# Optimization experiments

Measured on AMD Instinct MI355X. Metric: run time of the kernel, lower is better.

## Reference

```python
import jax, jax.numpy as jnp
import numpy as np

N = 100000   # nodes
E = 1600000  # edges
G = 512      # graphs in batch
F_IN = 30
H = 128
EPS = 1e-5   # BatchNorm1d default eps


def setup_inputs() -> dict:
    key = jax.random.key(0)
    ks = jax.random.split(key, 16)
    x = jax.random.normal(ks[0], (N, F_IN), dtype=jnp.float32)
    edge_index = jax.random.randint(ks[1], (2, E), 0, N, dtype=jnp.int64)
    batch = jnp.sort(jax.random.randint(ks[2], (N,), 0, G, dtype=jnp.int64))
    d = {"x": x, "edge_index": edge_index, "batch": batch}
    dims = [(F_IN, H), (H, H), (H, H)]
    for i, (din, dout) in enumerate(dims):
        d[f"W{i}"] = jax.random.normal(ks[3 + i], (din, dout), dtype=jnp.float32) * (1.0 / np.sqrt(din))
        d[f"b{i}"] = jnp.zeros((dout,), dtype=jnp.float32)
        d[f"g{i}"] = jnp.ones((dout,), dtype=jnp.float32)   # BN gamma
        d[f"bt{i}"] = jnp.zeros((dout,), dtype=jnp.float32)  # BN beta
    d["HW1"] = jax.random.normal(ks[9], (H, 64), dtype=jnp.float32) * (1.0 / np.sqrt(H))
    d["Hb1"] = jnp.zeros((64,), dtype=jnp.float32)
    d["HW2"] = jax.random.normal(ks[10], (64, 1), dtype=jnp.float32) * 0.125
    d["Hb2"] = jnp.zeros((1,), dtype=jnp.float32)
    return d


def _bn(x, gamma, beta):
    # training-mode BatchNorm1d over node dim, biased variance (as torch uses for normalization)
    mu = jnp.mean(x, axis=0)
    var = jnp.mean(jnp.square(x - mu), axis=0)
    return (x - mu) * jax.lax.rsqrt(var + EPS) * gamma + beta


def reference(x, edge_index, batch, W0, b0, g0, bt0, W1, b1, g1, bt1, W2, b2, g2, bt2, HW1, Hb1, HW2, Hb2):
    # GCNConv: add self-loops, symmetric D^{-1/2}(A+I)D^{-1/2} normalization
    loop = jnp.arange(N, dtype=edge_index.dtype)
    src = jnp.concatenate([edge_index[0], loop])  # [E+N]
    dst = jnp.concatenate([edge_index[1], loop])
    deg = jax.ops.segment_sum(jnp.ones(src.shape, jnp.float32), dst, num_segments=N)
    dinv = jax.lax.rsqrt(jnp.maximum(deg, 1.0))  # deg >= 1 due to self-loops
    norm = (dinv[src] * dinv[dst])[:, None]      # [E+N, 1]

    for W, b, g, bt in ((W0, b0, g0, bt0), (W1, b1, g1, bt1), (W2, b2, g2, bt2)):
        h = x @ W                                           # [N, H]
        agg = jax.ops.segment_sum(h[src] * norm, dst, num_segments=N) + b
        x = jnp.maximum(_bn(agg, g, bt), 0.0)               # BN + ReLU (dropout = identity here)

    # global_mean_pool over graph ids
    counts = jax.ops.segment_sum(jnp.ones((N,), jnp.float32), batch, num_segments=G)
    pooled = jax.ops.segment_sum(x, batch, num_segments=G) / jnp.maximum(counts, 1.0)[:, None]

    h = jnp.maximum(pooled @ HW1 + Hb1, 0.0)
    return (h @ HW2 + Hb2).squeeze(-1)  # [G]
```

## Files before the change

### kernel.cpp

```cpp
#include <hip/hip_runtime.h>

#define BN_EPS 1e-5f
#define BSH 8

typedef __attribute__((ext_vector_type(8))) short bf16x8;
typedef __attribute__((ext_vector_type(4))) float f32x4;

__device__ inline float bfhi(unsigned int v) { return __uint_as_float(v & 0xFFFF0000u); }
__device__ inline float bflo(unsigned int v) { return __uint_as_float(v << 16); }
__device__ inline unsigned short f2bf(float f) {
  unsigned int u = __float_as_uint(f);
  u += 0x7FFFu + ((u >> 16) & 1u);
  return (unsigned short)(u >> 16);
}
__device__ inline unsigned int pack2bf(float lo, float hi) {
  return (unsigned int)f2bf(lo) | ((unsigned int)f2bf(hi) << 16);
}

__global__ void k_prep(const int* __restrict__ src, const int* __restrict__ dst,
                       int* __restrict__ gcur, uint2* __restrict__ sedge,
                       int NB, int CAP, int E, int BB,
                       const float* __restrict__ x, const float* __restrict__ W0,
                       const float* __restrict__ W1, const float* __restrict__ W2,
                       unsigned short* __restrict__ xb, unsigned short* __restrict__ Wt0,
                       unsigned short* __restrict__ Wt1, unsigned short* __restrict__ Wt2,
                       int n) {
  if ((int)blockIdx.x < BB) {
    __shared__ int lh[512], rb[512];
    int tid = threadIdx.x;
    for (int i = tid; i < NB; i += 256) lh[i] = 0;
    __syncthreads();
    int base = blockIdx.x * 8192;
    int lim = min(8192, E - base);
    for (int i = tid; i < lim; i += 256)
      atomicAdd(&lh[dst[base + i] >> BSH], 1);
    __syncthreads();
    for (int i = tid; i < NB; i += 256) {
      int c = lh[i];
      rb[i] = c ? atomicAdd(&gcur[i], c) : 0;
      lh[i] = 0;
    }
    __syncthreads();
    for (int i = tid; i < lim; i += 256) {
      int d = dst[base + i];
      int s = src[base + i];
      int b = d >> BSH;
      int pos = rb[b] + atomicAdd(&lh[b], 1);
      if (pos < CAP) {
        uint2 v; v.x = (unsigned int)s; v.y = (unsigned int)d;
        sedge[(size_t)b * CAP + pos] = v;
      }
    }
  } else {
    int t0 = (((int)blockIdx.x - BB) * 256 + (int)threadIdx.x) * 4;
#pragma unroll
    for (int u = 0; u < 4; ++u) {
      int t = t0 + u;
      if (t < 4096) {
        int nn = t >> 5, k = t & 31;
        Wt0[t] = f2bf(k < 30 ? W0[k * 128 + nn] : 0.f);
      } else if (t < 20480) {
        int i = t - 4096; int nn = i >> 7, k = i & 127;
        Wt1[i] = f2bf(W1[k * 128 + nn]);
      } else if (t < 36864) {
        int i = t - 20480; int nn = i >> 7, k = i & 127;
        Wt2[i] = f2bf(W2[k * 128 + nn]);
      } else {
        int i = t - 36864;
        if (i < n * 32) {
          int row = i >> 5, c = i & 31;
          xb[i] = f2bf(c < 30 ? x[row * 30 + c] : 0.f);
        }
      }
    }
  }
}

__global__ void k_csr1(const uint2* __restrict__ sedge, const int* __restrict__ gcur,
                       int* __restrict__ startv, int* __restrict__ cnt,
                       float* __restrict__ dinv, int CAP, int n) {
  int b = blockIdx.x, tid = threadIdx.x;
  __shared__ int h[256], sc[256];
  h[tid] = 0;
  __syncthreads();
  int cb = gcur[b]; if (cb > CAP) cb = CAP;
  const uint2* sd = sedge + (size_t)b * CAP;
  for (int i = tid; i < cb; i += 256) atomicAdd(&h[sd[i].y & 255], 1);
  __syncthreads();
  int v = h[tid];
  sc[tid] = v;
  __syncthreads();
  for (int o = 1; o < 256; o <<= 1) {
    int t = (tid >= o) ? sc[tid - o] : 0;
    __syncthreads();
    sc[tid] += t;
    __syncthreads();
  }
  int gd = (b << BSH) + tid;
  if (gd < n) {
    startv[gd] = b * CAP + (sc[tid] - v);
    cnt[gd] = v;
    dinv[gd] = rsqrtf((float)v + 1.0f);
  }
}

__global__ void k_csr2(const uint2* __restrict__ sedge, const int* __restrict__ gcur,
                       const int* __restrict__ startv, const float* __restrict__ dinv,
                       unsigned int* __restrict__ elist, int CAP, int n) {
  int b = blockIdx.x, tid = threadIdx.x;
  __shared__ int cur[256];
  int gd = (b << BSH) + tid;
  cur[tid] = (gd < n) ? startv[gd] : 0;
  __syncthreads();
  int cb = gcur[b]; if (cb > CAP) cb = CAP;
  const uint2* sd = sedge + (size_t)b * CAP;
  for (int i = tid; i < cb; i += 256) {
    uint2 e = sd[i];
    int pos = atomicAdd(&cur[e.y & 255], 1);
    unsigned int u = (unsigned int)(dinv[e.x] * 32767.0f + 0.5f);
    elist[pos] = e.x | (u << 17);
  }
}

__global__ void k_gather0(const unsigned int* __restrict__ elist, const int* __restrict__ start,
                          const int* __restrict__ cnt, const float* __restrict__ dinv,
                          const uint4* __restrict__ x4,
                          unsigned int* __restrict__ G0, int n) {
  int lane = threadIdx.x & 63;
  int wv   = threadIdx.x >> 6;
  int grp  = lane >> 2;
  int q4   = lane & 3;
  int row  = blockIdx.x * 4 + wv;
  bool active = row < n;

  float acc[8];
  float di = 0.f, dq = 0.f;
  int len = 0;
  const unsigned int* ep = elist;
  if (active) {
    di = dinv[row];
    dq = di * (1.0f / 32767.0f);
    len = cnt[row];
    ep = elist + start[row];
  }
  {
    float selfw = (grp == 0 && active) ? di * di : 0.f;
    uint4 hv = (grp == 0 && active) ? x4[(size_t)row * 4 + q4] : make_uint4(0, 0, 0, 0);
    acc[0] = bflo(hv.x) * selfw; acc[1] = bfhi(hv.x) * selfw;
    acc[2] = bflo(hv.y) * selfw; acc[3] = bfhi(hv.y) * selfw;
    acc[4] = bflo(hv.z) * selfw; acc[5] = bfhi(hv.z) * selfw;
    acc[6] = bflo(hv.w) * selfw; acc[7] = bfhi(hv.w) * selfw;
  }
  for (int j = 0; j < len; j += 16) {
    int jj = j + grp;
    unsigned int e = (jj < len) ? ep[jj] : 0u;
    uint4 v = x4[(size_t)(e & 0x1FFFFu) * 4 + q4];
    float w = (float)(e >> 17) * dq;
    acc[0] = fmaf(bflo(v.x), w, acc[0]); acc[1] = fmaf(bfhi(v.x), w, acc[1]);
    acc[2] = fmaf(bflo(v.y), w, acc[2]); acc[3] = fmaf(bfhi(v.y), w, acc[3]);
    acc[4] = fmaf(bflo(v.z), w, acc[4]); acc[5] = fmaf(bfhi(v.z), w, acc[5]);
    acc[6] = fmaf(bflo(v.w), w, acc[6]); acc[7] = fmaf(bfhi(v.w), w, acc[7]);
  }
#pragma unroll
  for (int k = 0; k < 8; ++k) {
    acc[k] += __shfl_xor(acc[k], 4);
    acc[k] += __shfl_xor(acc[k], 8);
    acc[k] += __shfl_xor(acc[k], 16);
    acc[k] += __shfl_xor(acc[k], 32);
  }
  if (grp == 0 && active) {
    uint4 o;
    o.x = pack2bf(acc[0], acc[1]);
    o.y = pack2bf(acc[2], acc[3]);
    o.z = pack2bf(acc[4], acc[5]);
    o.w = pack2bf(acc[6], acc[7]);
    ((uint4*)G0)[(size_t)row * 4 + q4] = o;
  }
}

__global__ void k_gemm_mfma(const unsigned short* __restrict__ A,
                            const unsigned short* __restrict__ Wt,
                            const float* __restrict__ bnIn, const float* __restrict__ gamma,
                            const float* __restrict__ beta, int doBN,
                            const float* __restrict__ bias, float* __restrict__ bnslab,
                            int doStats, unsigned short* __restrict__ C, int n, int Kp) {
  __shared__ float ssc[128], ssh[128];
  if (doBN) {
    __shared__ float red[256];
    int tid = threadIdx.x;
    int which = tid >> 7, c = tid & 127;
    float s = 0.f;
    for (int k = 0; k < 64; ++k) s += bnIn[k * 256 + which * 128 + c];
    red[tid] = s;
    __syncthreads();
    if (tid < 128) {
      float invn = 1.0f / (float)n;
      float mu  = red[tid] * invn;
      float var = fmaxf(red[128 + tid] * invn - mu * mu, 0.f);
      float sc  = gamma[tid] * rsqrtf(var + BN_EPS);
      ssc[tid] = sc;
      ssh[tid] = fmaf(-mu, sc, beta[tid]);
    }
    __syncthreads();
  }
  int wave = threadIdx.x >> 6;
  int lane = threadIdx.x & 63;
  int m0 = blockIdx.x * 128 + wave * 32;
  int lm = lane & 15;
  int lq = lane >> 4;

  f32x4 acc[2][8] = {};
  const unsigned short* Arow0 = A + (size_t)(m0 + lm) * Kp + lq * 8;
  const unsigned short* Arow1 = Arow0 + (size_t)16 * Kp;
  const unsigned short* Bbase = Wt + (size_t)lm * Kp + lq * 8;

  for (int k0 = 0; k0 < Kp; k0 += 32) {
    uint4 ra0 = *(const uint4*)(Arow0 + k0);
    uint4 ra1 = *(const uint4*)(Arow1 + k0);
    bf16x8 a0, a1;
    if (doBN) {
      int cb = k0 + lq * 8;
      unsigned int w0 = pack2bf(fmaxf(fmaf(bflo(ra0.x), ssc[cb+0], ssh[cb+0]), 0.f),
                                fmaxf(fmaf(bfhi(ra0.x), ssc[cb+1], ssh[cb+1]), 0.f));
      unsigned int w1 = pack2bf(fmaxf(fmaf(bflo(ra0.y), ssc[cb+2], ssh[cb+2]), 0.f),
                                fmaxf(fmaf(bfhi(ra0.y), ssc[cb+3], ssh[cb+3]), 0.f));
      unsigned int w2 = pack2bf(fmaxf(fmaf(bflo(ra0.z), ssc[cb+4], ssh[cb+4]), 0.f),
                                fmaxf(fmaf(bfhi(ra0.z), ssc[cb+5], ssh[cb+5]), 0.f));
      unsigned int w3 = pack2bf(fmaxf(fmaf(bflo(ra0.w), ssc[cb+6], ssh[cb+6]), 0.f),
                                fmaxf(fmaf(bfhi(ra0.w), ssc[cb+7], ssh[cb+7]), 0.f));
      uint4 pa0 = make_uint4(w0, w1, w2, w3);
      a0 = *(bf16x8*)&pa0;
      unsigned int y0 = pack2bf(fmaxf(fmaf(bflo(ra1.x), ssc[cb+0], ssh[cb+0]), 0.f),
                                fmaxf(fmaf(bfhi(ra1.x), ssc[cb+1], ssh[cb+1]), 0.f));
      unsigned int y1 = pack2bf(fmaxf(fmaf(bflo(ra1.y), ssc[cb+2], ssh[cb+2]), 0.f),
                                fmaxf(fmaf(bfhi(ra1.y), ssc[cb+3], ssh[cb+3]), 0.f));
      unsigned int y2 = pack2bf(fmaxf(fmaf(bflo(ra1.z), ssc[cb+4], ssh[cb+4]), 0.f),
                                fmaxf(fmaf(bfhi(ra1.z), ssc[cb+5], ssh[cb+5]), 0.f));
      unsigned int y3 = pack2bf(fmaxf(fmaf(bflo(ra1.w), ssc[cb+6], ssh[cb+6]), 0.f),
                                fmaxf(fmaf(bfhi(ra1.w), ssc[cb+7], ssh[cb+7]), 0.f));
      uint4 pa1 = make_uint4(y0, y1, y2, y3);
      a1 = *(bf16x8*)&pa1;
    } else {
      a0 = *(bf16x8*)&ra0;
      a1 = *(bf16x8*)&ra1;
    }
#pragma unroll
    for (int t = 0; t < 8; ++t) {
      bf16x8 b = *(const bf16x8*)(Bbase + (size_t)t * 16 * Kp + k0);
      acc[0][t] = __builtin_amdgcn_mfma_f32_16x16x32_bf16(a0, b, acc[0][t], 0, 0, 0);
      acc[1][t] = __builtin_amdgcn_mfma_f32_16x16x32_bf16(a1, b, acc[1][t], 0, 0, 0);
    }
  }

#pragma unroll
  for (int h = 0; h < 2; ++h) {
    int rbase = m0 + h * 16 + lq * 4;
#pragma unroll
    for (int t = 0; t < 8; ++t) {
      int col = t * 16 + lm;
      float bv = doStats ? bias[col] : 0.f;
#pragma unroll
      for (int r = 0; r < 4; ++r) {
        int row = rbase + r;
        if (row < n) C[(size_t)row * 128 + col] = f2bf(acc[h][t][r] + bv);
      }
    }
  }

  if (doStats) {
    __shared__ float sms[4][256];
#pragma unroll
    for (int t = 0; t < 8; ++t) {
      int col = t * 16 + lm;
      float bv = bias[col];
      float s = 0.f, s2 = 0.f;
#pragma unroll
      for (int h = 0; h < 2; ++h) {
        int rbase = m0 + h * 16 + lq * 4;
#pragma unroll
        for (int r = 0; r < 4; ++r) {
          if (rbase + r < n) {
            float v = acc[h][t][r] + bv;
            s += v; s2 = fmaf(v, v, s2);
          }
        }
      }
      s  += __shfl_xor(s, 16);  s  += __shfl_xor(s, 32);
      s2 += __shfl_xor(s2, 16); s2 += __shfl_xor(s2, 32);
      if (lq == 0) { sms[wave][col] = s; sms[wave][128 + col] = s2; }
    }
    __syncthreads();
    int tid = threadIdx.x;
    int slab = (blockIdx.x & 63) * 256;
    float tot = sms[0][tid] + sms[1][tid] + sms[2][tid] + sms[3][tid];
    atomicAdd(&bnslab[slab + tid], tot);
  }
}

__global__ void k_gather(const unsigned int* __restrict__ elist, const int* __restrict__ start,
                         const int* __restrict__ cnt, const float* __restrict__ dinv,
                         const uint4* __restrict__ h4,
                         const float* __restrict__ bias, unsigned int* __restrict__ agg,
                         float* __restrict__ bnsumP, int n) {
  int lane = threadIdx.x & 63;
  int wv   = threadIdx.x >> 6;
  int grp  = lane >> 4;
  int c8   = lane & 15;
  int row  = blockIdx.x * 4 + wv;
  bool active = row < n;

  float acc[8];
  float di = 0.f, dq = 0.f;
  int len = 0;
  const unsigned int* ep = elist;

  if (active) {
    di = dinv[row];
    dq = di * (1.0f / 32767.0f);
    len = cnt[row];
    ep = elist + start[row];
  }

  {
    float selfw = (grp == 0 && active) ? di * di : 0.f;
    float4 b0 = make_float4(0.f, 0.f, 0.f, 0.f), b1 = b0;
    if (grp == 0 && active) {
      b0 = ((const float4*)bias)[c8 * 2];
      b1 = ((const float4*)bias)[c8 * 2 + 1];
    }
    uint4 hv = active ? h4[(size_t)row * 16 + c8] : make_uint4(0, 0, 0, 0);
    acc[0] = fmaf(bflo(hv.x), selfw, b0.x);
    acc[1] = fmaf(bfhi(hv.x), selfw, b0.y);
    acc[2] = fmaf(bflo(hv.y), selfw, b0.z);
    acc[3] = fmaf(bfhi(hv.y), selfw, b0.w);
    acc[4] = fmaf(bflo(hv.z), selfw, b1.x);
    acc[5] = fmaf(bfhi(hv.z), selfw, b1.y);
    acc[6] = fmaf(bflo(hv.w), selfw, b1.z);
    acc[7] = fmaf(bfhi(hv.w), selfw, b1.w);
  }

  int j = 0;
  for (; j + 8 <= len; j += 8) {
    unsigned int e0 = ep[j + grp];
    unsigned int e1 = ep[j + 4 + grp];
    uint4 v0 = h4[(size_t)(e0 & 0x1FFFFu) * 16 + c8];
    uint4 v1 = h4[(size_t)(e1 & 0x1FFFFu) * 16 + c8];
    float w0 = (float)(e0 >> 17) * dq;
    float w1 = (float)(e1 >> 17) * dq;
    acc[0] = fmaf(bflo(v0.x), w0, acc[0]); acc[1] = fmaf(bfhi(v0.x), w0, acc[1]);
    acc[2] = fmaf(bflo(v0.y), w0, acc[2]); acc[3] = fmaf(bfhi(v0.y), w0, acc[3]);
    acc[4] = fmaf(bflo(v0.z), w0, acc[4]); acc[5] = fmaf(bfhi(v0.z), w0, acc[5]);
    acc[6] = fmaf(bflo(v0.w), w0, acc[6]); acc[7] = fmaf(bfhi(v0.w), w0, acc[7]);
    acc[0] = fmaf(bflo(v1.x), w1, acc[0]); acc[1] = fmaf(bfhi(v1.x), w1, acc[1]);
    acc[2] = fmaf(bflo(v1.y), w1, acc[2]); acc[3] = fmaf(bfhi(v1.y), w1, acc[3]);
    acc[4] = fmaf(bflo(v1.z), w1, acc[4]); acc[5] = fmaf(bfhi(v1.z), w1, acc[5]);
    acc[6] = fmaf(bflo(v1.w), w1, acc[6]); acc[7] = fmaf(bfhi(v1.w), w1, acc[7]);
  }
  for (; j < len; j += 4) {
    int jj = j + grp;
    unsigned int e = (jj < len) ? ep[jj] : 0u;
    uint4 v = h4[(size_t)(e & 0x1FFFFu) * 16 + c8];
    float w = (float)(e >> 17) * dq;
    acc[0] = fmaf(bflo(v.x), w, acc[0]); acc[1] = fmaf(bfhi(v.x), w, acc[1]);
    acc[2] = fmaf(bflo(v.y), w, acc[2]); acc[3] = fmaf(bfhi(v.y), w, acc[3]);
    acc[4] = fmaf(bflo(v.z), w, acc[4]); acc[5] = fmaf(bfhi(v.z), w, acc[5]);
    acc[6] = fmaf(bflo(v.w), w, acc[6]); acc[7] = fmaf(bfhi(v.w), w, acc[7]);
  }

#pragma unroll
  for (int k = 0; k < 8; ++k) {
    acc[k] += __shfl_xor(acc[k], 16);
    acc[k] += __shfl_xor(acc[k], 32);
  }

  __shared__ float sm[2][4][128];
  if (lane < 16) {
    if (active) {
      uint4 o;
      o.x = pack2bf(acc[0], acc[1]);
      o.y = pack2bf(acc[2], acc[3]);
      o.z = pack2bf(acc[4], acc[5]);
      o.w = pack2bf(acc[6], acc[7]);
      ((uint4*)agg)[(size_t)row * 16 + c8] = o;
    }
#pragma unroll
    for (int k = 0; k < 8; ++k) {
      float a = acc[k];
      sm[0][wv][c8 * 8 + k] = a;
      sm[1][wv][c8 * 8 + k] = a * a;
    }
  }
  __syncthreads();
  int tid = threadIdx.x;
  int slab = (blockIdx.x & 63) * 256;
  if (tid < 128) {
    float s = sm[0][0][tid] + sm[0][1][tid] + sm[0][2][tid] + sm[0][3][tid];
    atomicAdd(&bnsumP[slab + tid], s);
  } else {
    int c = tid - 128;
    float s = sm[1][0][c] + sm[1][1][c] + sm[1][2][c] + sm[1][3][c];
    atomicAdd(&bnsumP[slab + 128 + c], s);
  }
}

__global__ void k_poolhead(const unsigned int* __restrict__ aggd, const float* __restrict__ bnIn,
                           const float* __restrict__ gamma, const float* __restrict__ beta,
                           const int* __restrict__ batch, const float* __restrict__ HW1,
                           const float* __restrict__ Hb1, const float* __restrict__ HW2,
                           const float* __restrict__ Hb2, float* __restrict__ out, int n) {
  __shared__ float bsc[128], bsh[128];
  {
    __shared__ float red[256];
    int tid = threadIdx.x;
    int which = tid >> 7, c = tid & 127;
    float s = 0.f;
    for (int k = 0; k < 64; ++k) s += bnIn[k * 256 + which * 128 + c];
    red[tid] = s;
    __syncthreads();
    if (tid < 128) {
      float invn = 1.0f / (float)n;
      float mu  = red[tid] * invn;
      float var = fmaxf(red[128 + tid] * invn - mu * mu, 0.f);
      float sc  = gamma[tid] * rsqrtf(var + BN_EPS);
      bsc[tid] = sc;
      bsh[tid] = fmaf(-mu, sc, beta[tid]);
    }
    __syncthreads();
  }
  int g = blockIdx.x;
  int wv = threadIdx.x >> 6, t = threadIdx.x & 63;
  int lo = 0, hi = n;
  while (lo < hi) { int mid = (lo + hi) >> 1; if (batch[mid] < g) lo = mid + 1; else hi = mid; }
  int s = lo;
  lo = 0; hi = n;
  int g1 = g + 1;
  while (lo < hi) { int mid = (lo + hi) >> 1; if (batch[mid] < g1) lo = mid + 1; else hi = mid; }
  int e = lo;

  float sc0 = bsc[2 * t], sc1 = bsc[2 * t + 1];
  float sh0 = bsh[2 * t], sh1 = bsh[2 * t + 1];
  float a0 = 0.f, a1 = 0.f;
  for (int i = s + wv; i < e; i += 4) {
    unsigned int u = aggd[(size_t)i * 64 + t];
    a0 += fmaxf(fmaf(bflo(u), sc0, sh0), 0.f);
    a1 += fmaxf(fmaf(bfhi(u), sc1, sh1), 0.f);
  }
  __shared__ float pp[4][128];
  pp[wv][2 * t] = a0;
  pp[wv][2 * t + 1] = a1;
  __syncthreads();
  if (wv == 0) {
    float inv = 1.0f / fmaxf((float)(e - s), 1.f);
    float p0 = (pp[0][2 * t] + pp[1][2 * t] + pp[2][2 * t] + pp[3][2 * t]) * inv;
    float p1 = (pp[0][2 * t + 1] + pp[1][2 * t + 1] + pp[2][2 * t + 1] + pp[3][2 * t + 1]) * inv;
    pp[0][2 * t] = p0;
    pp[0][2 * t + 1] = p1;
    float acc = Hb1[t];
    for (int k = 0; k < 128; ++k) acc = fmaf(pp[0][k], HW1[k * 64 + t], acc);
    float v = fmaxf(acc, 0.f) * HW2[t];
    for (int off = 32; off > 0; off >>= 1) v += __shfl_down(v, off);
    if (t == 0) out[g] = v + Hb2[0];
  }
}

extern "C" void kernel_launch(void* const* d_in, const int* in_sizes, int n_in,
                              void* d_out, int out_size, void* d_ws, size_t ws_size,
                              hipStream_t stream) {
  const int F_IN = 30, H = 128;
  const float* x   = (const float*)d_in[0];
  const int* eidx  = (const int*)d_in[1];
  const int* batch = (const int*)d_in[2];
  const int N = in_sizes[0] / F_IN;
  const int E = in_sizes[1] / 2;
  const int G = out_size;
  const int* srcp = eidx;
  const int* dstp = eidx + E;
  const float* HW1 = (const float*)d_in[15];
  const float* Hb1 = (const float*)d_in[16];
  const float* HW2 = (const float*)d_in[17];
  const float* Hb2 = (const float*)d_in[18];
  float* outp = (float*)d_out;

  const int Npad = (N + 127) & ~127;
  size_t nh = (size_t)Npad * H;
  const int NB = (N + 255) >> BSH;
  const int CAP = ((E / NB) * 3) / 2 + 128;
  const int NBpad = (NB + 63) & ~63;

  unsigned short* bufH = (unsigned short*)d_ws;
  unsigned short* bufX = bufH + nh;
  unsigned short* xbf  = bufX + nh;
  unsigned short* G0   = xbf + (size_t)Npad * 32;
  float* dinv = (float*)(G0 + (size_t)Npad * 32);
  int*   cnt    = (int*)(dinv + N);
  int*   startv = cnt + N;
  int*   gcur   = startv + N;
  float* bnsumP = (float*)(gcur + NBpad);
  unsigned short* Wt0 = (unsigned short*)(bnsumP + 3 * 64 * 256);
  unsigned short* Wt1 = Wt0 + 128 * 32;
  unsigned short* Wt2 = Wt1 + 128 * 128;
  unsigned int* elist = (unsigned int*)(Wt2 + 128 * 128 + 64);
  uint2* sedge = (uint2*)bufX;

  hipMemsetAsync(gcur, 0, ((size_t)NBpad + 3 * 64 * 256) * sizeof(int), stream);

  const int BB = (E + 8191) / 8192;
  const int TT = 36864 + N * 32;
  const int CV = (TT + 1023) >> 10;
  k_prep<<<BB + CV, 256, 0, stream>>>(srcp, dstp, gcur, sedge, NB, CAP, E, BB,
                                      x, (const float*)d_in[3], (const float*)d_in[7],
                                      (const float*)d_in[11], xbf, Wt0, Wt1, Wt2, N);
  k_csr1<<<NB, 256, 0, stream>>>(sedge, gcur, startv, cnt, dinv, CAP, N);
  k_csr2<<<NB, 256, 0, stream>>>(sedge, gcur, startv, dinv, elist, CAP, N);

  const float* b0  = (const float*)d_in[4];
  const float* gm0 = (const float*)d_in[5];
  const float* bt0 = (const float*)d_in[6];
  const float* b1  = (const float*)d_in[8];
  const float* gm1 = (const float*)d_in[9];
  const float* bt1 = (const float*)d_in[10];
  const float* b2  = (const float*)d_in[12];
  const float* gm2 = (const float*)d_in[13];
  const float* bt2 = (const float*)d_in[14];

  float* slab0 = bnsumP;
  float* slab1 = bnsumP + (size_t)1 * 64 * 256;
  float* slab2 = bnsumP + (size_t)2 * 64 * 256;

  k_gather0<<<(N + 3) / 4, 256, 0, stream>>>(elist, startv, cnt, dinv,
                                             (const uint4*)xbf, (unsigned int*)G0, N);
  k_gemm_mfma<<<Npad / 128, 256, 0, stream>>>(G0, Wt0, nullptr, nullptr, nullptr, 0,
                                              b0, slab0, 1, bufX, N, 32);

  k_gemm_mfma<<<Npad / 128, 256, 0, stream>>>(bufX, Wt1, slab0, gm0, bt0, 1,
                                              nullptr, nullptr, 0, bufH, N, 128);
  k_gather<<<(N + 3) / 4, 256, 0, stream>>>(elist, startv, cnt, dinv,
                                            (const uint4*)bufH, b1,
                                            (unsigned int*)bufX, slab1, N);

  k_gemm_mfma<<<Npad / 128, 256, 0, stream>>>(bufX, Wt2, slab1, gm1, bt1, 1,
                                              nullptr, nullptr, 0, bufH, N, 128);
  k_gather<<<(N + 3) / 4, 256, 0, stream>>>(elist, startv, cnt, dinv,
                                            (const uint4*)bufH, b2,
                                            (unsigned int*)bufX, slab2, N);

  k_poolhead<<<G, 256, 0, stream>>>((const unsigned int*)bufX, slab2, gm2, bt2, batch,
                                    HW1, Hb1, HW2, Hb2, outp, N);
}
```

Before: 448.4 us.

## Build CSR via global degree atomics and direct fill instead of bucketed sort

Replaces the two-pass bucketed edge sort (local histogram, staging buffer, per-bucket scan) with global per-node degree atomics, a per-block scan that claims its offset with an atomic tail counter, and a direct fill kernel using global atomic cursors. This drops the intermediate staging buffer traffic and the CAP overflow risk, at the cost of heavy global atomic contention and non-deterministic edge order within rows. The pooling kernel is also changed to read 8-byte vectors covering four channels, with two rows per wave and a shuffle reduction.

```diff
diff --git a/kernel.cpp b/kernel.cpp
--- a/kernel.cpp
+++ b/kernel.cpp
@@ -1,7 +1,6 @@
 #include <hip/hip_runtime.h>
 
 #define BN_EPS 1e-5f
-#define BSH 8
 
 typedef __attribute__((ext_vector_type(8))) short bf16x8;
 typedef __attribute__((ext_vector_type(4))) float f32x4;
@@ -17,42 +16,19 @@
   return (unsigned int)f2bf(lo) | ((unsigned int)f2bf(hi) << 16);
 }
 
-__global__ void k_prep(const int* __restrict__ src, const int* __restrict__ dst,
-                       int* __restrict__ gcur, uint2* __restrict__ sedge,
-                       int NB, int CAP, int E, int BB,
+__global__ void k_prep(const int* __restrict__ dst, int* __restrict__ cnt, int E, int BC,
                        const float* __restrict__ x, const float* __restrict__ W0,
                        const float* __restrict__ W1, const float* __restrict__ W2,
                        unsigned short* __restrict__ xb, unsigned short* __restrict__ Wt0,
                        unsigned short* __restrict__ Wt1, unsigned short* __restrict__ Wt2,
                        int n) {
-  if ((int)blockIdx.x < BB) {
-    __shared__ int lh[512], rb[512];
-    int tid = threadIdx.x;
-    for (int i = tid; i < NB; i += 256) lh[i] = 0;
-    __syncthreads();
+  if ((int)blockIdx.x < BC) {
     int base = blockIdx.x * 8192;
     int lim = min(8192, E - base);
-    for (int i = tid; i < lim; i += 256)
-      atomicAdd(&lh[dst[base + i] >> BSH], 1);
-    __syncthreads();
-    for (int i = tid; i < NB; i += 256) {
-      int c = lh[i];
-      rb[i] = c ? atomicAdd(&gcur[i], c) : 0;
-      lh[i] = 0;
-    }
-    __syncthreads();
-    for (int i = tid; i < lim; i += 256) {
-      int d = dst[base + i];
-      int s = src[base + i];
-      int b = d >> BSH;
-      int pos = rb[b] + atomicAdd(&lh[b], 1);
-      if (pos < CAP) {
-        uint2 v; v.x = (unsigned int)s; v.y = (unsigned int)d;
-        sedge[(size_t)b * CAP + pos] = v;
-      }
-    }
+    for (int i = threadIdx.x; i < lim; i += 256)
+      atomicAdd(&cnt[dst[base + i]], 1);
   } else {
-    int t0 = (((int)blockIdx.x - BB) * 256 + (int)threadIdx.x) * 4;
+    int t0 = (((int)blockIdx.x - BC) * 256 + (int)threadIdx.x) * 4;
 #pragma unroll
     for (int u = 0; u < 4; ++u) {
       int t = t0 + u;
@@ -76,18 +52,13 @@
   }
 }
 
-__global__ void k_csr1(const uint2* __restrict__ sedge, const int* __restrict__ gcur,
-                       int* __restrict__ startv, int* __restrict__ cnt,
-                       float* __restrict__ dinv, int CAP, int n) {
-  int b = blockIdx.x, tid = threadIdx.x;
-  __shared__ int h[256], sc[256];
-  h[tid] = 0;
-  __syncthreads();
-  int cb = gcur[b]; if (cb > CAP) cb = CAP;
-  const uint2* sd = sedge + (size_t)b * CAP;
-  for (int i = tid; i < cb; i += 256) atomicAdd(&h[sd[i].y & 255], 1);
-  __syncthreads();
-  int v = h[tid];
+__global__ void k_offsets(const int* __restrict__ cnt, int* __restrict__ startv,
+                          int* __restrict__ cur, float* __restrict__ dinv,
+                          int* __restrict__ tail, int n) {
+  int tid = threadIdx.x;
+  int gd = blockIdx.x * 256 + tid;
+  int v = (gd < n) ? cnt[gd] : 0;
+  __shared__ int sc[256];
   sc[tid] = v;
   __syncthreads();
   for (int o = 1; o < 256; o <<= 1) {
@@ -96,29 +67,30 @@
     sc[tid] += t;
     __syncthreads();
   }
-  int gd = (b << BSH) + tid;
+  __shared__ int base;
+  if (tid == 255) base = atomicAdd(tail, sc[255]);
+  __syncthreads();
   if (gd < n) {
-    startv[gd] = b * CAP + (sc[tid] - v);
-    cnt[gd] = v;
+    int st = base + sc[tid] - v;
+    startv[gd] = st;
+    cur[gd] = st;
     dinv[gd] = rsqrtf((float)v + 1.0f);
   }
 }
 
-__global__ void k_csr2(const uint2* __restrict__ sedge, const int* __restrict__ gcur,
-                       const int* __restrict__ startv, const float* __restrict__ dinv,
-                       unsigned int* __restrict__ elist, int CAP, int n) {
-  int b = blockIdx.x, tid = threadIdx.x;
-  __shared__ int cur[256];
-  int gd = (b << BSH) + tid;
-  cur[tid] = (gd < n) ? startv[gd] : 0;
-  __syncthreads();
-  int cb = gcur[b]; if (cb > CAP) cb = CAP;
-  const uint2* sd = sedge + (size_t)b * CAP;
-  for (int i = tid; i < cb; i += 256) {
-    uint2 e = sd[i];
-    int pos = atomicAdd(&cur[e.y & 255], 1);
-    unsigned int u = (unsigned int)(dinv[e.x] * 32767.0f + 0.5f);
-    elist[pos] = e.x | (u << 17);
+__global__ void k_fill(const int* __restrict__ src, const int* __restrict__ dst,
+                       int* __restrict__ cur, const float* __restrict__ dinv,
+                       unsigned int* __restrict__ elist, int E) {
+  int base = blockIdx.x * 1024;
+#pragma unroll
+  for (int u = 0; u < 4; ++u) {
+    int i = base + u * 256 + (int)threadIdx.x;
+    if (i < E) {
+      int d = dst[i], s = src[i];
+      int pos = atomicAdd(&cur[d], 1);
+      unsigned int q = (unsigned int)(dinv[s] * 32767.0f + 0.5f);
+      elist[pos] = (unsigned int)s | (q << 17);
+    }
   }
 }
 
@@ -437,17 +409,31 @@
   while (lo < hi) { int mid = (lo + hi) >> 1; if (batch[mid] < g1) lo = mid + 1; else hi = mid; }
   int e = lo;
 
-  float sc0 = bsc[2 * t], sc1 = bsc[2 * t + 1];
-  float sh0 = bsh[2 * t], sh1 = bsh[2 * t + 1];
-  float a0 = 0.f, a1 = 0.f;
-  for (int i = s + wv; i < e; i += 4) {
-    unsigned int u = aggd[(size_t)i * 64 + t];
-    a0 += fmaxf(fmaf(bflo(u), sc0, sh0), 0.f);
-    a1 += fmaxf(fmaf(bfhi(u), sc1, sh1), 0.f);
-  }
+  int c16 = t & 31;
+  int rpar = t >> 5;
+  float sc0 = bsc[4 * c16], sc1 = bsc[4 * c16 + 1];
+  float sc2 = bsc[4 * c16 + 2], sc3 = bsc[4 * c16 + 3];
+  float sh0 = bsh[4 * c16], sh1 = bsh[4 * c16 + 1];
+  float sh2 = bsh[4 * c16 + 2], sh3 = bsh[4 * c16 + 3];
+  float a0 = 0.f, a1 = 0.f, a2 = 0.f, a3 = 0.f;
+  for (int i = s + wv * 2 + rpar; i < e; i += 8) {
+    uint2 u = ((const uint2*)aggd)[(size_t)i * 32 + c16];
+    a0 += fmaxf(fmaf(bflo(u.x), sc0, sh0), 0.f);
+    a1 += fmaxf(fmaf(bfhi(u.x), sc1, sh1), 0.f);
+    a2 += fmaxf(fmaf(bflo(u.y), sc2, sh2), 0.f);
+    a3 += fmaxf(fmaf(bfhi(u.y), sc3, sh3), 0.f);
+  }
+  a0 += __shfl_xor(a0, 32);
+  a1 += __shfl_xor(a1, 32);
+  a2 += __shfl_xor(a2, 32);
+  a3 += __shfl_xor(a3, 32);
   __shared__ float pp[4][128];
-  pp[wv][2 * t] = a0;
-  pp[wv][2 * t + 1] = a1;
+  if (t < 32) {
+    pp[wv][4 * c16]     = a0;
+    pp[wv][4 * c16 + 1] = a1;
+    pp[wv][4 * c16 + 2] = a2;
+    pp[wv][4 * c16 + 3] = a3;
+  }
   __syncthreads();
   if (wv == 0) {
     float inv = 1.0f / fmaxf((float)(e - s), 1.f);
@@ -483,35 +469,32 @@
 
   const int Npad = (N + 127) & ~127;
   size_t nh = (size_t)Npad * H;
-  const int NB = (N + 255) >> BSH;
-  const int CAP = ((E / NB) * 3) / 2 + 128;
-  const int NBpad = (NB + 63) & ~63;
 
   unsigned short* bufH = (unsigned short*)d_ws;
   unsigned short* bufX = bufH + nh;
   unsigned short* xbf  = bufX + nh;
   unsigned short* G0   = xbf + (size_t)Npad * 32;
-  float* dinv = (float*)(G0 + (size_t)Npad * 32);
-  int*   cnt    = (int*)(dinv + N);
-  int*   startv = cnt + N;
-  int*   gcur   = startv + N;
-  float* bnsumP = (float*)(gcur + NBpad);
+  float* dinv   = (float*)(G0 + (size_t)Npad * 32);
+  int*   startv = (int*)(dinv + N);
+  int*   cur    = startv + N;
+  int*   cnt    = cur + N;
+  int*   tail   = cnt + N;
+  float* bnsumP = (float*)(tail + 64);
   unsigned short* Wt0 = (unsigned short*)(bnsumP + 3 * 64 * 256);
   unsigned short* Wt1 = Wt0 + 128 * 32;
   unsigned short* Wt2 = Wt1 + 128 * 128;
   unsigned int* elist = (unsigned int*)(Wt2 + 128 * 128 + 64);
-  uint2* sedge = (uint2*)bufX;
-
-  hipMemsetAsync(gcur, 0, ((size_t)NBpad + 3 * 64 * 256) * sizeof(int), stream);
-
-  const int BB = (E + 8191) / 8192;
+
+  hipMemsetAsync(cnt, 0, ((size_t)N + 64 + 3 * 64 * 256) * sizeof(int), stream);
+
+  const int BC = (E + 8191) / 8192;
   const int TT = 36864 + N * 32;
   const int CV = (TT + 1023) >> 10;
-  k_prep<<<BB + CV, 256, 0, stream>>>(srcp, dstp, gcur, sedge, NB, CAP, E, BB,
+  k_prep<<<BC + CV, 256, 0, stream>>>(dstp, cnt, E, BC,
                                       x, (const float*)d_in[3], (const float*)d_in[7],
                                       (const float*)d_in[11], xbf, Wt0, Wt1, Wt2, N);
-  k_csr1<<<NB, 256, 0, stream>>>(sedge, gcur, startv, cnt, dinv, CAP, N);
-  k_csr2<<<NB, 256, 0, stream>>>(sedge, gcur, startv, dinv, elist, CAP, N);
+  k_offsets<<<(N + 255) / 256, 256, 0, stream>>>(cnt, startv, cur, dinv, tail, N);
+  k_fill<<<(E + 1023) / 1024, 256, 0, stream>>>(srcp, dstp, cur, dinv, elist, E);
 
   const float* b0  = (const float*)d_in[4];
   const float* gm0 = (const float*)d_in[5];
```

Result: slower. 576.2 us (+28.5%).
